# Optimization experiments

Measured on AMD Instinct MI355X. Metric: run time of the kernel, lower is better.

Reference implementation:

```python
import jax, jax.numpy as jnp
import numpy as np

N, M_CODES, Z_DIM = 4096, 4096, 1024


def setup_inputs() -> dict:
    key = jax.random.key(0)
    k1, k2 = jax.random.split(key)
    z = jax.random.normal(k1, (N, Z_DIM), dtype=jnp.float32)
    e = jax.random.normal(k2, (M_CODES, Z_DIM), dtype=jnp.float32)
    return {"z": z, "e": e}


def reference(z, e):
    # Squared pairwise L2 distances [N, M] via GEMM expansion:
    # ||z_i - e_j||^2 = ||z_i||^2 + ||e_j||^2 - 2 z_i . e_j
    z_sq = jnp.sum(z * z, axis=1)               # [N]
    e_sq = jnp.sum(e * e, axis=1)               # [M]
    cross = jnp.einsum('nd,md->nm', z, e)       # [N, M]
    dist = z_sq[:, None] + e_sq[None, :] - 2.0 * cross  # [N, M]
    # min over dim 0 (over data points N) -> per-code nearest distance [M]
    loss = jnp.mean(jnp.min(dist, axis=0))
    return loss
```

## Files before the change

kernel.cpp:

```cpp
#include <hip/hip_runtime.h>
#include <hip/hip_bf16.h>
#include <stdint.h>

#define N_PTS   4096
#define M_CODES 4096
#define ZDIM    1024
#define BM 128
#define BN 128
#define BK 32

typedef __attribute__((ext_vector_type(8))) short bf16x8;
typedef __attribute__((ext_vector_type(4))) float f32x4;

__device__ __forceinline__ unsigned short f2bf(float f) {
    __hip_bfloat16 h = __float2bfloat16(f);
    return *reinterpret_cast<unsigned short*>(&h);
}

__device__ __forceinline__ unsigned enc_f32(float f) {
    unsigned u = __float_as_uint(f);
    return (u & 0x80000000u) ? ~u : (u | 0x80000000u);
}
__device__ __forceinline__ float dec_f32(unsigned e) {
    unsigned u = (e & 0x80000000u) ? (e ^ 0x80000000u) : ~e;
    return __uint_as_float(u);
}

__global__ __launch_bounds__(256) void prep_kernel(
    const float* __restrict__ z, const float* __restrict__ e,
    unsigned short* __restrict__ zb, unsigned short* __restrict__ eb,
    float* __restrict__ zsq, float* __restrict__ esq,
    unsigned* __restrict__ min_enc) {
    const int row = blockIdx.x;
    const int t = threadIdx.x;
    if (row < 16) min_enc[row * 256 + t] = 0xFFFFFFFFu;

    const float* src;
    unsigned short* dst;
    float* sqp;
    if (row < N_PTS) {
        src = z + (size_t)row * ZDIM; dst = zb + (size_t)row * ZDIM; sqp = zsq + row;
    } else {
        const int r = row - N_PTS;
        src = e + (size_t)r * ZDIM; dst = eb + (size_t)r * ZDIM; sqp = esq + r;
    }
    float4 v = reinterpret_cast<const float4*>(src)[t];
    ushort4 o;
    o.x = f2bf(v.x); o.y = f2bf(v.y); o.z = f2bf(v.z); o.w = f2bf(v.w);
    reinterpret_cast<ushort4*>(dst)[t] = o;
    float s = v.x * v.x + v.y * v.y + v.z * v.z + v.w * v.w;
    #pragma unroll
    for (int off = 32; off > 0; off >>= 1) s += __shfl_down(s, off, 64);
    __shared__ float red[4];
    if ((t & 63) == 0) red[t >> 6] = s;
    __syncthreads();
    if (t == 0) *sqp = red[0] + red[1] + red[2] + red[3];
}

__global__ __launch_bounds__(256) void gemm_min_kernel(
    const unsigned short* __restrict__ zb, const unsigned short* __restrict__ eb,
    const float* __restrict__ zsq, unsigned* __restrict__ min_enc) {
    __shared__ __align__(16) unsigned short As[BM * BK];
    __shared__ __align__(16) unsigned short Bs[BN * BK];
    __shared__ float zsq_s[BM];

    const int t = threadIdx.x;
    const int bx = blockIdx.x;
    const int by = blockIdx.y;
    const int lane = t & 63;
    const int w = t >> 6;
    const int wm = w >> 1, wn = w & 1;
    const int lrow = lane & 15;
    const int q = lane >> 4;

    if (t < BM) zsq_s[t] = zsq[by * BM + t];

    f32x4 acc[4][4];
    #pragma unroll
    for (int i = 0; i < 4; i++)
        #pragma unroll
        for (int j = 0; j < 4; j++) acc[i][j] = (f32x4){0.f, 0.f, 0.f, 0.f};

    const int row0 = (t * 16) >> 6;
    const int kel0 = ((t * 16) & 63) >> 1;
    const int lds_b0 = (t >> 6) * 512;
    const size_t a_base = (size_t)(by * BM) * ZDIM;
    const size_t b_base = (size_t)(bx * BN) * ZDIM;

    for (int k0 = 0; k0 < ZDIM; k0 += BK) {
        const unsigned short* ga0 = zb + a_base + (size_t)row0 * ZDIM + k0 + kel0;
        const unsigned short* gb0 = eb + b_base + (size_t)row0 * ZDIM + k0 + kel0;
        __builtin_amdgcn_global_load_lds(
            (const __attribute__((address_space(1))) void*)ga0,
            (__attribute__((address_space(3))) void*)(As + lds_b0), 16, 0, 0);
        __builtin_amdgcn_global_load_lds(
            (const __attribute__((address_space(1))) void*)(ga0 + (size_t)64 * ZDIM),
            (__attribute__((address_space(3))) void*)(As + 2048 + lds_b0), 16, 0, 0);
        __builtin_amdgcn_global_load_lds(
            (const __attribute__((address_space(1))) void*)gb0,
            (__attribute__((address_space(3))) void*)(Bs + lds_b0), 16, 0, 0);
        __builtin_amdgcn_global_load_lds(
            (const __attribute__((address_space(1))) void*)(gb0 + (size_t)64 * ZDIM),
            (__attribute__((address_space(3))) void*)(Bs + 2048 + lds_b0), 16, 0, 0);
        __syncthreads();

        bf16x8 a[4], b[4];
        #pragma unroll
        for (int am = 0; am < 4; am++)
            a[am] = *(const bf16x8*)(As + (wm * 64 + am * 16 + lrow) * BK + q * 8);
        #pragma unroll
        for (int an = 0; an < 4; an++)
            b[an] = *(const bf16x8*)(Bs + (wn * 64 + an * 16 + lrow) * BK + q * 8);
        #pragma unroll
        for (int am = 0; am < 4; am++)
            #pragma unroll
            for (int an = 0; an < 4; an++)
                acc[am][an] = __builtin_amdgcn_mfma_f32_16x16x32_bf16(
                    a[am], b[an], acc[am][an], 0, 0, 0);
        __syncthreads();
    }

    #pragma unroll
    for (int an = 0; an < 4; an++) {
        float v = 3.4e38f;
        #pragma unroll
        for (int am = 0; am < 4; am++) {
            const int rbase = wm * 64 + am * 16 + q * 4;
            f32x4 c = acc[am][an];
            v = fminf(v, zsq_s[rbase + 0] - 2.f * c[0]);
            v = fminf(v, zsq_s[rbase + 1] - 2.f * c[1]);
            v = fminf(v, zsq_s[rbase + 2] - 2.f * c[2]);
            v = fminf(v, zsq_s[rbase + 3] - 2.f * c[3]);
        }
        v = fminf(v, __shfl_xor(v, 16, 64));
        v = fminf(v, __shfl_xor(v, 32, 64));
        if (q == 0) {
            const int col = bx * BN + wn * 64 + an * 16 + lrow;
            atomicMin(&min_enc[col], enc_f32(v));
        }
    }
}

__global__ __launch_bounds__(256) void finalize_kernel(
    const unsigned* __restrict__ min_enc, const float* __restrict__ esq,
    float* __restrict__ out) {
    const int t = threadIdx.x;
    float s = 0.f;
    #pragma unroll
    for (int i = 0; i < M_CODES / 256; i++) {
        const int j = i * 256 + t;
        s += dec_f32(min_enc[j]) + esq[j];
    }
    #pragma unroll
    for (int off = 32; off > 0; off >>= 1) s += __shfl_down(s, off, 64);
    __shared__ float red[4];
    if ((t & 63) == 0) red[t >> 6] = s;
    __syncthreads();
    if (t == 0) out[0] = (red[0] + red[1] + red[2] + red[3]) * (1.f / M_CODES);
}

extern "C" void kernel_launch(void* const* d_in, const int* in_sizes, int n_in,
                              void* d_out, int out_size, void* d_ws, size_t ws_size,
                              hipStream_t stream) {
    (void)in_sizes; (void)n_in; (void)out_size; (void)ws_size;
    const float* z = (const float*)d_in[0];
    const float* e = (const float*)d_in[1];
    char* ws = (char*)d_ws;
    unsigned short* zb = (unsigned short*)ws;
    unsigned short* eb = (unsigned short*)(ws + ((size_t)8 << 20));
    float* zsq = (float*)(ws + ((size_t)16 << 20));
    float* esq = (float*)(ws + ((size_t)16 << 20) + 4096 * 4);
    unsigned* min_enc = (unsigned*)(ws + ((size_t)16 << 20) + 2 * 4096 * 4);

    prep_kernel<<<dim3(8192), dim3(256), 0, stream>>>(z, e, zb, eb, zsq, esq, min_enc);
    gemm_min_kernel<<<dim3(M_CODES / BN, N_PTS / BM), dim3(256), 0, stream>>>(
        zb, eb, zsq, min_enc);
    finalize_kernel<<<dim3(1), dim3(256), 0, stream>>>(min_enc, esq, (float*)d_out);
}
```

Measured before the change: 125.0 us.

## Fuse prep, GEMM-min and finalize into one persistent kernel with grid barrier

Merges the bf16 conversion/norm kernel, the GEMM column-min kernel and the finalize kernel into a single launch of 1024 blocks. A software grid barrier on an atomic counter separates the conversion phase from the GEMM, and the last block to finish performs the final reduction. The e-norms are collapsed into one atomically accumulated scalar, and per-block column minima are combined in shared memory before a single atomicMin per column. This targets launch overhead and redundant atomics, but relies on all 1024 blocks being co-resident (launch bounds request 4 blocks per SIMD group) and adds the spin-wait and two memset launches.

```diff
diff --git a/kernel.cpp b/kernel.cpp
--- a/kernel.cpp
+++ b/kernel.cpp
@@ -8,6 +8,7 @@
 #define BM 128
 #define BN 128
 #define BK 32
+#define GRID    ((N_PTS / BM) * (M_CODES / BN))
 
 typedef __attribute__((ext_vector_type(8))) short bf16x8;
 typedef __attribute__((ext_vector_type(4))) float f32x4;
@@ -26,49 +27,64 @@
     return __uint_as_float(u);
 }
 
-__global__ __launch_bounds__(256) void prep_kernel(
+__global__ __launch_bounds__(256, 4) void fused_kernel(
     const float* __restrict__ z, const float* __restrict__ e,
     unsigned short* __restrict__ zb, unsigned short* __restrict__ eb,
-    float* __restrict__ zsq, float* __restrict__ esq,
-    unsigned* __restrict__ min_enc) {
-    const int row = blockIdx.x;
-    const int t = threadIdx.x;
-    if (row < 16) min_enc[row * 256 + t] = 0xFFFFFFFFu;
-
-    const float* src;
-    unsigned short* dst;
-    float* sqp;
-    if (row < N_PTS) {
-        src = z + (size_t)row * ZDIM; dst = zb + (size_t)row * ZDIM; sqp = zsq + row;
-    } else {
-        const int r = row - N_PTS;
-        src = e + (size_t)r * ZDIM; dst = eb + (size_t)r * ZDIM; sqp = esq + r;
-    }
-    float4 v = reinterpret_cast<const float4*>(src)[t];
-    ushort4 o;
-    o.x = f2bf(v.x); o.y = f2bf(v.y); o.z = f2bf(v.z); o.w = f2bf(v.w);
-    reinterpret_cast<ushort4*>(dst)[t] = o;
-    float s = v.x * v.x + v.y * v.y + v.z * v.z + v.w * v.w;
-    #pragma unroll
-    for (int off = 32; off > 0; off >>= 1) s += __shfl_down(s, off, 64);
-    __shared__ float red[4];
-    if ((t & 63) == 0) red[t >> 6] = s;
-    __syncthreads();
-    if (t == 0) *sqp = red[0] + red[1] + red[2] + red[3];
-}
-
-__global__ __launch_bounds__(256) void gemm_min_kernel(
-    const unsigned short* __restrict__ zb, const unsigned short* __restrict__ eb,
-    const float* __restrict__ zsq, unsigned* __restrict__ min_enc) {
+    float* __restrict__ zsq, unsigned* __restrict__ min_enc,
+    unsigned* __restrict__ ctrl,
+    float* __restrict__ out) {
     __shared__ __align__(16) unsigned short As[BM * BK];
     __shared__ __align__(16) unsigned short Bs[BN * BK];
     __shared__ float zsq_s[BM];
+    __shared__ float colmin[2][BN];
+    __shared__ float red[4];
+    __shared__ int last_flag;
 
     const int t = threadIdx.x;
-    const int bx = blockIdx.x;
-    const int by = blockIdx.y;
+    const int b = blockIdx.x;
     const int lane = t & 63;
     const int w = t >> 6;
+
+    #pragma unroll
+    for (int r = 0; r < 2; r++) {
+        const int row = b * 8 + w * 2 + r;
+        const bool is_z = row < N_PTS;
+        const int rr = is_z ? row : row - N_PTS;
+        const float* src = (is_z ? z : e) + (size_t)rr * ZDIM;
+        unsigned short* dst = (is_z ? zb : eb) + (size_t)rr * ZDIM;
+        const float4* s4 = reinterpret_cast<const float4*>(src);
+        ushort4* d4 = reinterpret_cast<ushort4*>(dst);
+        float s = 0.f;
+        #pragma unroll
+        for (int i = 0; i < 4; i++) {
+            float4 v = s4[i * 64 + lane];
+            ushort4 o;
+            o.x = f2bf(v.x); o.y = f2bf(v.y); o.z = f2bf(v.z); o.w = f2bf(v.w);
+            d4[i * 64 + lane] = o;
+            s += v.x * v.x + v.y * v.y + v.z * v.z + v.w * v.w;
+        }
+        #pragma unroll
+        for (int off = 1; off < 64; off <<= 1) s += __shfl_xor(s, off, 64);
+        if (lane == 0) {
+            if (is_z) zsq[rr] = s;
+            else atomicAdd((float*)&ctrl[2], s);
+        }
+    }
+
+    __threadfence();
+    __syncthreads();
+    if (t == 0) {
+        __hip_atomic_fetch_add(&ctrl[0], 1u, __ATOMIC_ACQ_REL,
+                               __HIP_MEMORY_SCOPE_AGENT);
+        while (__hip_atomic_load(&ctrl[0], __ATOMIC_ACQUIRE,
+                                 __HIP_MEMORY_SCOPE_AGENT) < (unsigned)GRID)
+            __builtin_amdgcn_s_sleep(8);
+    }
+    __syncthreads();
+    __threadfence();
+
+    const int bx = b & 31;
+    const int by = b >> 5;
     const int wm = w >> 1, wn = w & 1;
     const int lrow = lane & 15;
     const int q = lane >> 4;
@@ -83,7 +99,7 @@
 
     const int row0 = (t * 16) >> 6;
     const int kel0 = ((t * 16) & 63) >> 1;
-    const int lds_b0 = (t >> 6) * 512;
+    const int lds_b0 = w * 512;
     const size_t a_base = (size_t)(by * BM) * ZDIM;
     const size_t b_base = (size_t)(bx * BN) * ZDIM;
 
@@ -104,19 +120,19 @@
             (__attribute__((address_space(3))) void*)(Bs + 2048 + lds_b0), 16, 0, 0);
         __syncthreads();
 
-        bf16x8 a[4], b[4];
+        bf16x8 a[4], bb[4];
         #pragma unroll
         for (int am = 0; am < 4; am++)
             a[am] = *(const bf16x8*)(As + (wm * 64 + am * 16 + lrow) * BK + q * 8);
         #pragma unroll
         for (int an = 0; an < 4; an++)
-            b[an] = *(const bf16x8*)(Bs + (wn * 64 + an * 16 + lrow) * BK + q * 8);
+            bb[an] = *(const bf16x8*)(Bs + (wn * 64 + an * 16 + lrow) * BK + q * 8);
         #pragma unroll
         for (int am = 0; am < 4; am++)
             #pragma unroll
             for (int an = 0; an < 4; an++)
                 acc[am][an] = __builtin_amdgcn_mfma_f32_16x16x32_bf16(
-                    a[am], b[an], acc[am][an], 0, 0, 0);
+                    a[am], bb[an], acc[am][an], 0, 0, 0);
         __syncthreads();
     }
 
@@ -134,29 +150,43 @@
         }
         v = fminf(v, __shfl_xor(v, 16, 64));
         v = fminf(v, __shfl_xor(v, 32, 64));
-        if (q == 0) {
-            const int col = bx * BN + wn * 64 + an * 16 + lrow;
-            atomicMin(&min_enc[col], enc_f32(v));
-        }
-    }
-}
-
-__global__ __launch_bounds__(256) void finalize_kernel(
-    const unsigned* __restrict__ min_enc, const float* __restrict__ esq,
-    float* __restrict__ out) {
-    const int t = threadIdx.x;
-    float s = 0.f;
-    #pragma unroll
-    for (int i = 0; i < M_CODES / 256; i++) {
-        const int j = i * 256 + t;
-        s += dec_f32(min_enc[j]) + esq[j];
-    }
-    #pragma unroll
-    for (int off = 32; off > 0; off >>= 1) s += __shfl_down(s, off, 64);
-    __shared__ float red[4];
-    if ((t & 63) == 0) red[t >> 6] = s;
-    __syncthreads();
-    if (t == 0) out[0] = (red[0] + red[1] + red[2] + red[3]) * (1.f / M_CODES);
+        if (q == 0) colmin[wm][wn * 64 + an * 16 + lrow] = v;
+    }
+    __syncthreads();
+    if (t < BN) {
+        const float m = fminf(colmin[0][t], colmin[1][t]);
+        atomicMin(&min_enc[bx * BN + t], enc_f32(m));
+    }
+
+    __threadfence();
+    if (t == 0) {
+        unsigned old = __hip_atomic_fetch_add(&ctrl[1], 1u, __ATOMIC_ACQ_REL,
+                                              __HIP_MEMORY_SCOPE_AGENT);
+        last_flag = (old == (unsigned)(GRID - 1));
+    }
+    __syncthreads();
+    if (last_flag) {
+        __threadfence();
+        float s = 0.f;
+        #pragma unroll
+        for (int i = 0; i < M_CODES / 256; i++) {
+            const int j = i * 256 + t;
+            unsigned enc = __hip_atomic_load(&min_enc[j], __ATOMIC_RELAXED,
+                                             __HIP_MEMORY_SCOPE_AGENT);
+            s += dec_f32(enc);
+        }
+        #pragma unroll
+        for (int off = 1; off < 64; off <<= 1) s += __shfl_xor(s, off, 64);
+        if (lane == 0) red[w] = s;
+        __syncthreads();
+        if (t == 0) {
+            unsigned eb_bits = __hip_atomic_load(&ctrl[2], __ATOMIC_RELAXED,
+                                                 __HIP_MEMORY_SCOPE_AGENT);
+            float esq_total = __uint_as_float(eb_bits);
+            out[0] = (red[0] + red[1] + red[2] + red[3] + esq_total)
+                     * (1.f / M_CODES);
+        }
+    }
 }
 
 extern "C" void kernel_launch(void* const* d_in, const int* in_sizes, int n_in,
@@ -169,11 +199,11 @@
     unsigned short* zb = (unsigned short*)ws;
     unsigned short* eb = (unsigned short*)(ws + ((size_t)8 << 20));
     float* zsq = (float*)(ws + ((size_t)16 << 20));
-    float* esq = (float*)(ws + ((size_t)16 << 20) + 4096 * 4);
-    unsigned* min_enc = (unsigned*)(ws + ((size_t)16 << 20) + 2 * 4096 * 4);
-
-    prep_kernel<<<dim3(8192), dim3(256), 0, stream>>>(z, e, zb, eb, zsq, esq, min_enc);
-    gemm_min_kernel<<<dim3(M_CODES / BN, N_PTS / BM), dim3(256), 0, stream>>>(
-        zb, eb, zsq, min_enc);
-    finalize_kernel<<<dim3(1), dim3(256), 0, stream>>>(min_enc, esq, (float*)d_out);
-}
+    unsigned* min_enc = (unsigned*)(ws + ((size_t)16 << 20) + 16384);
+    unsigned* ctrl = (unsigned*)(ws + ((size_t)16 << 20) + 32768);
+
+    hipMemsetAsync(min_enc, 0xFF, M_CODES * sizeof(unsigned), stream);
+    hipMemsetAsync(ctrl, 0, 16, stream);
+    fused_kernel<<<dim3(GRID), dim3(256), 0, stream>>>(
+        z, e, zb, eb, zsq, min_enc, ctrl, (float*)d_out);
+}
```

New measurement: 467.0 us. 3.73x slower.
